# Optimization experiments

Hardware: AMD Instinct MI355X
Metric: run time of the kernel (lower is better)

## Reference

```python
import jax, jax.numpy as jnp
import numpy as np

N_ITERS = 3  # Set2Set n_iters


def _set2set(feat, gid, B, Wih, Whh, bih, bhh):
    # DGL Set2Set with n_iters=3, n_layers=1: LSTM(input=2D, hidden=D), PyTorch gate order i,f,g,o
    N, D = feat.shape
    q_star = jnp.zeros((B, 2 * D), feat.dtype)
    h = jnp.zeros((B, D), feat.dtype)
    c = jnp.zeros((B, D), feat.dtype)
    bias = bih + bhh
    for _ in range(N_ITERS):
        gates = q_star @ Wih.T + h @ Whh.T + bias  # (B, 4D)
        i, f, g, o = jnp.split(gates, 4, axis=-1)
        i = jax.nn.sigmoid(i); f = jax.nn.sigmoid(f); o = jax.nn.sigmoid(o); g = jnp.tanh(g)
        c = f * c + i * g
        h = o * jnp.tanh(c)  # q = h, shape (B, D)
        e = jnp.sum(feat * h[gid], axis=-1)  # (N,) attention logits
        m = jax.ops.segment_max(e, gid, num_segments=B, indices_are_sorted=True)
        ex = jnp.exp(e - m[gid])
        s = jax.ops.segment_sum(ex, gid, num_segments=B, indices_are_sorted=True)
        alpha = ex / s[gid]  # segment softmax
        readout = jax.ops.segment_sum(feat * alpha[:, None], gid, num_segments=B, indices_are_sorted=True)
        q_star = jnp.concatenate([h, readout], axis=-1)  # (B, 2D)
    return q_star


def setup_inputs() -> dict:
    key = jax.random.key(0)
    ks = jax.random.split(key, 18)
    N, E, D, B, OUT = 100000, 1000000, 64, 64, 1
    s = 1.0 / np.sqrt(D)
    u = lambda k, shp, b: jax.random.uniform(k, shp, jnp.float32, -b, b)
    inp = {
        'feat': jax.random.normal(ks[0], (N, D), jnp.float32),
        'efeat': jax.random.normal(ks[1], (E, D), jnp.float32),
        'edge_dst': jax.random.randint(ks[2], (E,), 0, N, jnp.int32),
        'node_graph': jnp.sort(jax.random.randint(ks[3], (N,), 0, B, jnp.int32)),
        'n_graphs': B,
        'node_Wih': u(ks[4], (4 * D, 2 * D), s), 'node_Whh': u(ks[5], (4 * D, D), s),
        'node_bih': u(ks[6], (4 * D,), s), 'node_bhh': u(ks[7], (4 * D,), s),
        'edge_Wih': u(ks[8], (4 * D, 2 * D), s), 'edge_Whh': u(ks[9], (4 * D, D), s),
        'edge_bih': u(ks[10], (4 * D,), s), 'edge_bhh': u(ks[11], (4 * D,), s),
        'W1': u(ks[12], (32, 4 * D), np.sqrt(6.0 / (4 * D + 32)) * np.sqrt(2.0)),
        'b1': jnp.zeros((32,), jnp.float32),
        'W2': u(ks[13], (16, 32), np.sqrt(6.0 / 48) * np.sqrt(2.0)),
        'b2': jnp.zeros((16,), jnp.float32),
        'W3': u(ks[14], (OUT, 16), np.sqrt(6.0 / (16 + OUT)) * np.sqrt(2.0)),
        'b3': jnp.zeros((OUT,), jnp.float32),
    }
    return inp


def reference(feat, efeat, edge_dst, node_graph, n_graphs,
              node_Wih, node_Whh, node_bih, node_bhh,
              edge_Wih, edge_Whh, edge_bih, edge_bhh,
              W1, b1, W2, b2, W3, b3):
    N = feat.shape[0]
    # mpnn = identity: node_emb = feat, edge_emb = efeat
    node_s2s = _set2set(feat, node_graph, n_graphs, node_Wih, node_Whh, node_bih, node_bhh)
    # graph.update_all(fn.copy_e, fn.mean): scatter-mean of edge features onto dst nodes
    deg = jax.ops.segment_sum(jnp.ones((efeat.shape[0],), feat.dtype), edge_dst, num_segments=N)
    edge_agg = jax.ops.segment_sum(efeat, edge_dst, num_segments=N) / jnp.maximum(deg, 1.0)[:, None]
    edge_s2s = _set2set(edge_agg, node_graph, n_graphs, edge_Wih, edge_Whh, edge_bih, edge_bhh)
    out = jnp.concatenate([node_s2s, edge_s2s], axis=1)  # (B, 4D)
    out = jax.nn.relu(out @ W1.T + b1)
    out = jax.nn.relu(out @ W2.T + b2)
    out = out @ W3.T + b3
    return out
```

## Files before the change

kernel.cpp:

```cpp
#include <hip/hip_runtime.h>
#include <math.h>

#define D 64
#define B 64
#define NPB 128
#define NSLOT 4
#define SCAN_BS 1024

__device__ __forceinline__ unsigned encf(float x) {
  unsigned u = __float_as_uint(x);
  return (u & 0x80000000u) ? ~u : (u | 0x80000000u);
}
__device__ __forceinline__ float decf(unsigned e) {
  return (e & 0x80000000u) ? __uint_as_float(e ^ 0x80000000u) : __uint_as_float(~e);
}
__device__ __forceinline__ float sigm(float x) { return 1.0f / (1.0f + __expf(-x)); }


__global__ void k_deg(const int* __restrict__ edge_dst, int* __restrict__ deg, int E) {
  int i = blockIdx.x * blockDim.x + threadIdx.x;
  if (i < E) atomicAdd(&deg[edge_dst[i]], 1);
}

__global__ void k_scan1(const int* __restrict__ deg, int* __restrict__ row_start,
                        int* __restrict__ blocksum, int N) {
  __shared__ int sm[SCAN_BS];
  int t = threadIdx.x;
  int base = blockIdx.x * SCAN_BS;
  int v = (base + t < N) ? deg[base + t] : 0;
  sm[t] = v;
  __syncthreads();
  for (int ofs = 1; ofs < SCAN_BS; ofs <<= 1) {
    int add = (t >= ofs) ? sm[t - ofs] : 0;
    __syncthreads();
    sm[t] += add;
    __syncthreads();
  }
  if (base + t < N) row_start[base + t] = sm[t] - v;
  if (t == SCAN_BS - 1) blocksum[blockIdx.x] = sm[t];
}

__global__ void k_scan2(int* __restrict__ blocksum, int nb) {
  __shared__ int sm[128];
  int t = threadIdx.x;
  int v = (t < nb) ? blocksum[t] : 0;
  sm[t] = v;
  __syncthreads();
  for (int ofs = 1; ofs < 128; ofs <<= 1) {
    int add = (t >= ofs) ? sm[t - ofs] : 0;
    __syncthreads();
    sm[t] += add;
    __syncthreads();
  }
  if (t < nb) blocksum[t] = sm[t] - v;
}

__global__ void k_scan3(int* __restrict__ row_start, const int* __restrict__ blocksum,
                        int* __restrict__ cursor, int N) {
  int n = blockIdx.x * blockDim.x + threadIdx.x;
  if (n < N) {
    int v = row_start[n] + blocksum[n / SCAN_BS];
    row_start[n] = v;
    cursor[n] = v;
  }
}

__global__ void k_fill(const int* __restrict__ edge_dst, int* __restrict__ cursor,
                       int* __restrict__ csr, int E) {
  int e = blockIdx.x * blockDim.x + threadIdx.x;
  if (e < E) {
    int dst = edge_dst[e];
    int idx = atomicAdd(&cursor[dst], 1);
    csr[idx] = e;
  }
}

__global__ void k_gather(const float* __restrict__ efeat, const int* __restrict__ csr,
                         const int* __restrict__ row_start, const int* __restrict__ deg,
                         float* __restrict__ edge_agg, int N) {
  int grp = (blockIdx.x * blockDim.x + threadIdx.x) >> 4;
  int l16 = threadIdx.x & 15;
  if (grp >= N) return;
  int base = row_start[grp];
  int dg = deg[grp];
  float4 acc = make_float4(0.f, 0.f, 0.f, 0.f);
  for (int i = 0; i < dg; i += 16) {
    int idx[16];
    #pragma unroll
    for (int j = 0; j < 16; ++j) {
      int k = i + j;
      idx[j] = csr[base + (k < dg ? k : dg - 1)];
    }
    #pragma unroll
    for (int j = 0; j < 16; ++j) {
      float4 v = *(const float4*)(efeat + (size_t)idx[j] * D + l16 * 4);
      bool ok = (i + j < dg);
      acc.x += ok ? v.x : 0.0f;
      acc.y += ok ? v.y : 0.0f;
      acc.z += ok ? v.z : 0.0f;
      acc.w += ok ? v.w : 0.0f;
    }
  }
  float inv = 1.0f / fmaxf((float)dg, 1.0f);
  acc.x *= inv; acc.y *= inv; acc.z *= inv; acc.w *= inv;
  *(float4*)(edge_agg + (size_t)grp * D + l16 * 4) = acc;
}


__global__ void k_lstm2(int first, float* __restrict__ h2, float* __restrict__ c2,
                        float* __restrict__ s2, float* __restrict__ r2,
                        unsigned* __restrict__ m2, float* __restrict__ off2,
                        const float* __restrict__ nWih, const float* __restrict__ nWhh,
                        const float* __restrict__ nbih, const float* __restrict__ nbhh,
                        const float* __restrict__ eWih, const float* __restrict__ eWhh,
                        const float* __restrict__ ebih, const float* __restrict__ ebhh) {
  __shared__ float sq[2 * D], sg[4 * D];
  int side = blockIdx.y;
  const float* Wih = side ? eWih : nWih;
  const float* Whh = side ? eWhh : nWhh;
  const float* bih = side ? ebih : nbih;
  const float* bhh = side ? ebhh : nbhh;
  float* h = h2 + side * B * D;
  float* c = c2 + side * B * D;
  float* s_buf = s2 + side * B;
  float* r_buf = r2 + side * B * D;

  int b = blockIdx.x, j = threadIdx.x;
  if (j < D) {
    sq[j] = h[b * D + j];
  } else if (j < 2 * D) {
    sq[j] = first ? 0.0f : (r_buf[b * D + (j - D)] / s_buf[b]);
  }
  __syncthreads();
  float acc = bih[j] + bhh[j];
  const float* wr = Wih + (size_t)j * (2 * D);
  #pragma unroll 8
  for (int k = 0; k < 2 * D; ++k) acc += sq[k] * wr[k];
  const float* wr2 = Whh + (size_t)j * D;
  #pragma unroll 8
  for (int k = 0; k < D; ++k) acc += sq[k] * wr2[k];
  sg[j] = acc;
  __syncthreads();
  if (j < D) {
    float ig = sigm(sg[j]);
    float fg = sigm(sg[D + j]);
    float gg = tanhf(sg[2 * D + j]);
    float og = sigm(sg[3 * D + j]);
    float cn = fg * c[b * D + j] + ig * gg;
    c[b * D + j] = cn;
    h[b * D + j] = og * tanhf(cn);
    r_buf[b * D + j] = 0.0f;
  }
  if (j == D) s_buf[b] = 0.0f;
  if (j == D + 1) {
    int idx = side * B + b;
    off2[idx] = first ? 0.0f : decf(m2[idx]);
    m2[idx] = 0u;
  }
}

__global__ void k_att_fused(const float* __restrict__ feat, const float* __restrict__ edge_agg,
                            const int* __restrict__ gid, const float* __restrict__ h2,
                            const float* __restrict__ off2, unsigned* __restrict__ m2,
                            float* __restrict__ s2, float* __restrict__ r2, int N) {
  __shared__ float r_lds[16 * NSLOT * D];
  __shared__ float s_lds[16 * NSLOT];
  __shared__ float m_lds[16 * NSLOT];
  __shared__ float h_lds[NSLOT * D];
  __shared__ float o_lds[NSLOT];
  __shared__ int sg_first;
  __shared__ int used[NSLOT];

  int side = blockIdx.y;
  const float* F = side ? edge_agg : feat;
  const float* h = h2 + side * B * D;
  const float* off = off2 + side * B;
  unsigned* m_enc = m2 + side * B;
  float* s_buf = s2 + side * B;
  float* r_buf = r2 + side * B * D;

  int tid = threadIdx.x;
  int grp = tid >> 4;
  int d4  = tid & 15;
  int base = blockIdx.x * NPB;

  for (int i = tid; i < 16 * NSLOT * D; i += 256) r_lds[i] = 0.0f;
  if (tid < 16 * NSLOT) { s_lds[tid] = 0.0f; m_lds[tid] = -3.4e38f; }
  if (tid < NSLOT) used[tid] = 0;
  if (tid == 0) sg_first = gid[base];
  __syncthreads();
  int gfirst = sg_first;
  {
    int slot = tid >> 6, dim = tid & 63;
    int g = gfirst + slot;
    if (g < B) {
      h_lds[tid] = h[g * D + dim];
      if (dim == 0) o_lds[slot] = off[g];
    }
  }
  __syncthreads();

  float4 acc = make_float4(0.f, 0.f, 0.f, 0.f);
  float sum_ex = 0.0f;
  float local_max = -3.4e38f;
  int cur_g = -1;

  for (int it = 0; it < NPB / 32; ++it) {
    int n0 = base + it * 32 + grp;
    int n1 = n0 + 16;
    bool ok0 = n0 < N, ok1 = n1 < N;
    int g0 = ok0 ? gid[n0] : -1;
    int g1 = ok1 ? gid[n1] : -1;
    float4 f0 = make_float4(0,0,0,0), f1 = make_float4(0,0,0,0);
    float dot0 = 0.f, dot1 = 0.f, ex0 = 0.f, ex1 = 0.f;
    if (ok0) {
      f0 = *(const float4*)(F + (size_t)n0 * D + d4 * 4);
      int s0 = g0 - gfirst;
      float4 hv = (s0 >= 0 && s0 < NSLOT) ? *(const float4*)&h_lds[(s0 << 6) + (d4 << 2)]
                                          : *(const float4*)(h + (size_t)g0 * D + d4 * 4);
      dot0 = f0.x * hv.x + f0.y * hv.y + f0.z * hv.z + f0.w * hv.w;
    }
    if (ok1) {
      f1 = *(const float4*)(F + (size_t)n1 * D + d4 * 4);
      int s1 = g1 - gfirst;
      float4 hv = (s1 >= 0 && s1 < NSLOT) ? *(const float4*)&h_lds[(s1 << 6) + (d4 << 2)]
                                          : *(const float4*)(h + (size_t)g1 * D + d4 * 4);
      dot1 = f1.x * hv.x + f1.y * hv.y + f1.z * hv.z + f1.w * hv.w;
    }
    dot0 += __shfl_xor(dot0, 1); dot1 += __shfl_xor(dot1, 1);
    dot0 += __shfl_xor(dot0, 2); dot1 += __shfl_xor(dot1, 2);
    dot0 += __shfl_xor(dot0, 4); dot1 += __shfl_xor(dot1, 4);
    dot0 += __shfl_xor(dot0, 8); dot1 += __shfl_xor(dot1, 8);
    if (ok0) {
      int s0 = g0 - gfirst;
      ex0 = __expf(dot0 - ((s0 >= 0 && s0 < NSLOT) ? o_lds[s0] : off[g0]));
    }
    if (ok1) {
      int s1 = g1 - gfirst;
      ex1 = __expf(dot1 - ((s1 >= 0 && s1 < NSLOT) ? o_lds[s1] : off[g1]));
    }

    #pragma unroll
    for (int pair = 0; pair < 2; ++pair) {
      bool ok = pair ? ok1 : ok0;
      int g = pair ? g1 : g0;
      float ex = pair ? ex1 : ex0;
      float dt = pair ? dot1 : dot0;
      float4 f = pair ? f1 : f0;
      if (!ok) continue;
      if (g != cur_g) {
        if (cur_g >= 0) {
          int slot = cur_g - gfirst;
          if (slot >= 0 && slot < NSLOT) {
            float4* p = (float4*)&r_lds[((grp * NSLOT + slot) << 6) + (d4 << 2)];
            float4 v = *p;
            v.x += acc.x; v.y += acc.y; v.z += acc.z; v.w += acc.w;
            *p = v;
            if (d4 == 0) {
              s_lds[grp * NSLOT + slot] += sum_ex;
              m_lds[grp * NSLOT + slot] = fmaxf(m_lds[grp * NSLOT + slot], local_max);
              used[slot] = 1;
            }
          } else {
            float* rp = r_buf + cur_g * D + d4 * 4;
            atomicAdd(rp + 0, acc.x); atomicAdd(rp + 1, acc.y);
            atomicAdd(rp + 2, acc.z); atomicAdd(rp + 3, acc.w);
            if (d4 == 0) { atomicAdd(&s_buf[cur_g], sum_ex); atomicMax(&m_enc[cur_g], encf(local_max)); }
          }
        }
        cur_g = g; acc = make_float4(0,0,0,0); sum_ex = 0.f; local_max = -3.4e38f;
      }
      acc.x += ex * f.x; acc.y += ex * f.y; acc.z += ex * f.z; acc.w += ex * f.w;
      if (d4 == 0) { sum_ex += ex; local_max = fmaxf(local_max, dt); }
    }
  }
  if (cur_g >= 0) {
    int slot = cur_g - gfirst;
    if (slot >= 0 && slot < NSLOT) {
      float4* p = (float4*)&r_lds[((grp * NSLOT + slot) << 6) + (d4 << 2)];
      float4 v = *p;
      v.x += acc.x; v.y += acc.y; v.z += acc.z; v.w += acc.w;
      *p = v;
      if (d4 == 0) {
        s_lds[grp * NSLOT + slot] += sum_ex;
        m_lds[grp * NSLOT + slot] = fmaxf(m_lds[grp * NSLOT + slot], local_max);
        used[slot] = 1;
      }
    } else {
      float* rp = r_buf + cur_g * D + d4 * 4;
      atomicAdd(rp + 0, acc.x); atomicAdd(rp + 1, acc.y);
      atomicAdd(rp + 2, acc.z); atomicAdd(rp + 3, acc.w);
      if (d4 == 0) { atomicAdd(&s_buf[cur_g], sum_ex); atomicMax(&m_enc[cur_g], encf(local_max)); }
    }
  }
  __syncthreads();

  {
    int slot = tid >> 6, dim = tid & 63;
    int g = gfirst + slot;
    if (g < B && used[slot]) {
      float sum = 0.0f;
      #pragma unroll
      for (int q = 0; q < 16; ++q) sum += r_lds[((q * NSLOT + slot) << 6) + dim];
      atomicAdd(&r_buf[g * D + dim], sum);
    }
  }
  if (tid < NSLOT) {
    int g = gfirst + tid;
    if (g < B && used[tid]) {
      float ssum = 0.0f;
      #pragma unroll
      for (int q = 0; q < 16; ++q) ssum += s_lds[q * NSLOT + tid];
      atomicAdd(&s_buf[g], ssum);
    }
  } else if (tid >= 64 && tid < 64 + NSLOT) {
    int slot = tid - 64;
    int g = gfirst + slot;
    if (g < B && used[slot]) {
      float mmax = -3.4e38f;
      #pragma unroll
      for (int q = 0; q < 16; ++q) mmax = fmaxf(mmax, m_lds[q * NSLOT + slot]);
      atomicMax(&m_enc[g], encf(mmax));
    }
  }
}

__global__ void k_mlp(const float* __restrict__ h2, const float* __restrict__ r2,
                      const float* __restrict__ s2,
                      const float* __restrict__ W1, const float* __restrict__ b1,
                      const float* __restrict__ W2, const float* __restrict__ b2,
                      const float* __restrict__ W3, const float* __restrict__ b3,
                      float* __restrict__ out) {
  __shared__ float x[4 * D], h1[32], h2s[16];
  int b = blockIdx.x, t = threadIdx.x;
  x[t]       = (t < D) ? h2[b * D + t]         : r2[b * D + (t - D)] / s2[b];
  x[128 + t] = (t < D) ? h2[B * D + b * D + t] : r2[B * D + b * D + (t - D)] / s2[B + b];
  __syncthreads();
  if (t < 32) {
    float acc = b1[t];
    const float* w = W1 + (size_t)t * (4 * D);
    #pragma unroll 8
    for (int k = 0; k < 4 * D; ++k) acc += x[k] * w[k];
    h1[t] = fmaxf(acc, 0.0f);
  }
  __syncthreads();
  if (t < 16) {
    float acc = b2[t];
    const float* w = W2 + (size_t)t * 32;
    #pragma unroll
    for (int k = 0; k < 32; ++k) acc += h1[k] * w[k];
    h2s[t] = fmaxf(acc, 0.0f);
  }
  __syncthreads();
  if (t == 0) {
    float acc = b3[0];
    #pragma unroll
    for (int k = 0; k < 16; ++k) acc += h2s[k] * W3[k];
    out[b] = acc;
  }
}


extern "C" void kernel_launch(void* const* d_in, const int* in_sizes, int n_in,
                              void* d_out, int out_size, void* d_ws, size_t ws_size,
                              hipStream_t stream) {
  const float* feat      = (const float*)d_in[0];
  const float* efeat     = (const float*)d_in[1];
  const int*   edge_dst  = (const int*)d_in[2];
  const int*   node_graph= (const int*)d_in[3];
  const float* node_Wih  = (const float*)d_in[5];
  const float* node_Whh  = (const float*)d_in[6];
  const float* node_bih  = (const float*)d_in[7];
  const float* node_bhh  = (const float*)d_in[8];
  const float* edge_Wih  = (const float*)d_in[9];
  const float* edge_Whh  = (const float*)d_in[10];
  const float* edge_bih  = (const float*)d_in[11];
  const float* edge_bhh  = (const float*)d_in[12];
  const float* W1 = (const float*)d_in[13];
  const float* b1 = (const float*)d_in[14];
  const float* W2 = (const float*)d_in[15];
  const float* b2 = (const float*)d_in[16];
  const float* W3 = (const float*)d_in[17];
  const float* b3 = (const float*)d_in[18];
  float* out = (float*)d_out;

  const int N = in_sizes[0] / D;
  const int E = in_sizes[2];

  float* ws = (float*)d_ws;
  size_t off = 0;
  float* edge_agg = ws + off; off += (size_t)N * D;
  float* h2       = ws + off; off += 2 * B * D;
  float* c2       = ws + off; off += 2 * B * D;
  float* s2       = ws + off; off += 2 * B;
  float* r2       = ws + off; off += 2 * B * D;
  float* off2     = ws + off; off += 2 * B;
  unsigned* m2    = (unsigned*)(ws + off); off += 2 * B;
  int* deg        = (int*)(ws + off); off += N;
  int* row_start  = (int*)(ws + off); off += N;
  int* cursor     = (int*)(ws + off); off += N;
  int* blocksum   = (int*)(ws + off); off += 128;
  int* csr        = (int*)(ws + off); off += E + 8;

  hipMemsetAsync(deg, 0, (size_t)N * sizeof(int), stream);
  hipMemsetAsync(h2, 0, (size_t)(4 * B * D) * sizeof(float), stream);

  const int nb = (N + SCAN_BS - 1) / SCAN_BS;
  k_deg<<<(E + 255) / 256, 256, 0, stream>>>(edge_dst, deg, E);
  k_scan1<<<nb, SCAN_BS, 0, stream>>>(deg, row_start, blocksum, N);
  k_scan2<<<1, 128, 0, stream>>>(blocksum, nb);
  k_scan3<<<(N + 255) / 256, 256, 0, stream>>>(row_start, blocksum, cursor, N);
  k_fill<<<(E + 255) / 256, 256, 0, stream>>>(edge_dst, cursor, csr, E);

  k_gather<<<(N + 15) / 16, 256, 0, stream>>>(efeat, csr, row_start, deg, edge_agg, N);

  const int att_blocks = (N + NPB - 1) / NPB;
  dim3 ga(att_blocks, 2), gb(B, 2);

  for (int it = 0; it < 3; ++it) {
    k_lstm2<<<gb, 256, 0, stream>>>(it == 0 ? 1 : 0, h2, c2, s2, r2, m2, off2,
                                    node_Wih, node_Whh, node_bih, node_bhh,
                                    edge_Wih, edge_Whh, edge_bih, edge_bhh);
    k_att_fused<<<ga, 256, 0, stream>>>(feat, edge_agg, node_graph, h2, off2, m2, s2, r2, N);
  }

  k_mlp<<<B, 128, 0, stream>>>(h2, r2, s2, W1, b1, W2, b2, W3, b3, out);
}
```

Before: 261.1 us.

## Switch edge aggregation to edge-parallel segmented reduction and fuse small setup kernels

```diff
diff --git a/kernel.cpp b/kernel.cpp
--- a/kernel.cpp
+++ b/kernel.cpp
@@ -6,6 +6,7 @@
 #define NPB 128
 #define NSLOT 4
 #define SCAN_BS 1024
+#define GR 128
 
 __device__ __forceinline__ unsigned encf(float x) {
   unsigned u = __float_as_uint(x);
@@ -17,105 +18,15 @@
 __device__ __forceinline__ float sigm(float x) { return 1.0f / (1.0f + __expf(-x)); }
 
 
-__global__ void k_deg(const int* __restrict__ edge_dst, int* __restrict__ deg, int E) {
-  int i = blockIdx.x * blockDim.x + threadIdx.x;
-  if (i < E) atomicAdd(&deg[edge_dst[i]], 1);
-}
-
-__global__ void k_scan1(const int* __restrict__ deg, int* __restrict__ row_start,
-                        int* __restrict__ blocksum, int N) {
-  __shared__ int sm[SCAN_BS];
-  int t = threadIdx.x;
-  int base = blockIdx.x * SCAN_BS;
-  int v = (base + t < N) ? deg[base + t] : 0;
-  sm[t] = v;
-  __syncthreads();
-  for (int ofs = 1; ofs < SCAN_BS; ofs <<= 1) {
-    int add = (t >= ofs) ? sm[t - ofs] : 0;
-    __syncthreads();
-    sm[t] += add;
-    __syncthreads();
-  }
-  if (base + t < N) row_start[base + t] = sm[t] - v;
-  if (t == SCAN_BS - 1) blocksum[blockIdx.x] = sm[t];
-}
-
-__global__ void k_scan2(int* __restrict__ blocksum, int nb) {
-  __shared__ int sm[128];
-  int t = threadIdx.x;
-  int v = (t < nb) ? blocksum[t] : 0;
-  sm[t] = v;
-  __syncthreads();
-  for (int ofs = 1; ofs < 128; ofs <<= 1) {
-    int add = (t >= ofs) ? sm[t - ofs] : 0;
-    __syncthreads();
-    sm[t] += add;
-    __syncthreads();
-  }
-  if (t < nb) blocksum[t] = sm[t] - v;
-}
-
-__global__ void k_scan3(int* __restrict__ row_start, const int* __restrict__ blocksum,
-                        int* __restrict__ cursor, int N) {
-  int n = blockIdx.x * blockDim.x + threadIdx.x;
-  if (n < N) {
-    int v = row_start[n] + blocksum[n / SCAN_BS];
-    row_start[n] = v;
-    cursor[n] = v;
-  }
-}
-
-__global__ void k_fill(const int* __restrict__ edge_dst, int* __restrict__ cursor,
-                       int* __restrict__ csr, int E) {
-  int e = blockIdx.x * blockDim.x + threadIdx.x;
-  if (e < E) {
-    int dst = edge_dst[e];
-    int idx = atomicAdd(&cursor[dst], 1);
-    csr[idx] = e;
-  }
-}
-
-__global__ void k_gather(const float* __restrict__ efeat, const int* __restrict__ csr,
-                         const int* __restrict__ row_start, const int* __restrict__ deg,
-                         float* __restrict__ edge_agg, int N) {
-  int grp = (blockIdx.x * blockDim.x + threadIdx.x) >> 4;
-  int l16 = threadIdx.x & 15;
-  if (grp >= N) return;
-  int base = row_start[grp];
-  int dg = deg[grp];
-  float4 acc = make_float4(0.f, 0.f, 0.f, 0.f);
-  for (int i = 0; i < dg; i += 16) {
-    int idx[16];
-    #pragma unroll
-    for (int j = 0; j < 16; ++j) {
-      int k = i + j;
-      idx[j] = csr[base + (k < dg ? k : dg - 1)];
-    }
-    #pragma unroll
-    for (int j = 0; j < 16; ++j) {
-      float4 v = *(const float4*)(efeat + (size_t)idx[j] * D + l16 * 4);
-      bool ok = (i + j < dg);
-      acc.x += ok ? v.x : 0.0f;
-      acc.y += ok ? v.y : 0.0f;
-      acc.z += ok ? v.z : 0.0f;
-      acc.w += ok ? v.w : 0.0f;
-    }
-  }
-  float inv = 1.0f / fmaxf((float)dg, 1.0f);
-  acc.x *= inv; acc.y *= inv; acc.z *= inv; acc.w *= inv;
-  *(float4*)(edge_agg + (size_t)grp * D + l16 * 4) = acc;
-}
-
-
-__global__ void k_lstm2(int first, float* __restrict__ h2, float* __restrict__ c2,
-                        float* __restrict__ s2, float* __restrict__ r2,
-                        unsigned* __restrict__ m2, float* __restrict__ off2,
-                        const float* __restrict__ nWih, const float* __restrict__ nWhh,
-                        const float* __restrict__ nbih, const float* __restrict__ nbhh,
-                        const float* __restrict__ eWih, const float* __restrict__ eWhh,
-                        const float* __restrict__ ebih, const float* __restrict__ ebhh) {
-  __shared__ float sq[2 * D], sg[4 * D];
-  int side = blockIdx.y;
+__device__ __forceinline__ void lstm_body(int side, int b, int first,
+    float* __restrict__ h2, float* __restrict__ c2,
+    float* __restrict__ s2, float* __restrict__ r2,
+    unsigned* __restrict__ m2, float* __restrict__ off2,
+    const float* __restrict__ nWih, const float* __restrict__ nWhh,
+    const float* __restrict__ nbih, const float* __restrict__ nbhh,
+    const float* __restrict__ eWih, const float* __restrict__ eWhh,
+    const float* __restrict__ ebih, const float* __restrict__ ebhh,
+    float* sq, float* sg) {
   const float* Wih = side ? eWih : nWih;
   const float* Whh = side ? eWhh : nWhh;
   const float* bih = side ? ebih : nbih;
@@ -125,7 +36,7 @@
   float* s_buf = s2 + side * B;
   float* r_buf = r2 + side * B * D;
 
-  int b = blockIdx.x, j = threadIdx.x;
+  int j = threadIdx.x;
   if (j < D) {
     sq[j] = h[b * D + j];
   } else if (j < 2 * D) {
@@ -158,6 +69,150 @@
     m2[idx] = 0u;
   }
 }
+
+
+__global__ void k_deg_lstm(int DEG, const int* __restrict__ edge_dst, int* __restrict__ deg, int E,
+                           float* __restrict__ h2, float* __restrict__ c2,
+                           float* __restrict__ s2, float* __restrict__ r2,
+                           unsigned* __restrict__ m2, float* __restrict__ off2,
+                           const float* __restrict__ nWih, const float* __restrict__ nWhh,
+                           const float* __restrict__ nbih, const float* __restrict__ nbhh,
+                           const float* __restrict__ eWih, const float* __restrict__ eWhh,
+                           const float* __restrict__ ebih, const float* __restrict__ ebhh) {
+  __shared__ float sq[2 * D], sg[4 * D];
+  int bx = blockIdx.x;
+  if (bx < DEG) {
+    int i = bx * 256 + threadIdx.x;
+    if (i < E) atomicAdd(&deg[edge_dst[i]], 1);
+  } else {
+    int j = bx - DEG;
+    lstm_body(j >> 6, j & 63, 1, h2, c2, s2, r2, m2, off2,
+              nWih, nWhh, nbih, nbhh, eWih, eWhh, ebih, ebhh, sq, sg);
+  }
+}
+
+__global__ void k_scan1(const int* __restrict__ deg, int* __restrict__ row_start,
+                        int* __restrict__ blocksum, int N) {
+  __shared__ int sm[SCAN_BS];
+  int t = threadIdx.x;
+  int base = blockIdx.x * SCAN_BS;
+  int v = (base + t < N) ? deg[base + t] : 0;
+  sm[t] = v;
+  __syncthreads();
+  for (int ofs = 1; ofs < SCAN_BS; ofs <<= 1) {
+    int add = (t >= ofs) ? sm[t - ofs] : 0;
+    __syncthreads();
+    sm[t] += add;
+    __syncthreads();
+  }
+  if (base + t < N) row_start[base + t] = sm[t] - v;
+  if (t == SCAN_BS - 1) blocksum[blockIdx.x] = sm[t];
+}
+
+__global__ void k_scan3(int* __restrict__ row_start, const int* __restrict__ blocksum,
+                        int* __restrict__ cursor, int N, int nb) {
+  __shared__ int sm[128];
+  int t = threadIdx.x;
+  if (t < 128) sm[t] = (t < nb) ? blocksum[t] : 0;
+  __syncthreads();
+  for (int ofs = 1; ofs < 128; ofs <<= 1) {
+    int add = (t < 128 && t >= ofs) ? sm[t - ofs] : 0;
+    __syncthreads();
+    if (t < 128) sm[t] += add;
+    __syncthreads();
+  }
+  int n = blockIdx.x * 256 + t;
+  if (n < N) {
+    int c = n / SCAN_BS;
+    int v = row_start[n] + ((c > 0) ? sm[c - 1] : 0);
+    row_start[n] = v;
+    cursor[n] = v;
+  }
+}
+
+__global__ void k_fill(const int* __restrict__ edge_dst, int* __restrict__ cursor,
+                       int* __restrict__ csr, int* __restrict__ csr_dst, int E) {
+  int e = blockIdx.x * blockDim.x + threadIdx.x;
+  if (e < E) {
+    int dst = edge_dst[e];
+    int idx = atomicAdd(&cursor[dst], 1);
+    csr[idx] = e;
+    csr_dst[idx] = dst;
+  }
+}
+
+__global__ void k_gather(const float* __restrict__ efeat, const int* __restrict__ csr,
+                         const int* __restrict__ csr_dst, float* __restrict__ edge_agg, int E) {
+  __shared__ int s_id[4 * GR], s_d[4 * GR];
+  int tid = threadIdx.x;
+  int bbase = blockIdx.x * (4 * GR);
+  #pragma unroll
+  for (int q = 0; q < 2; ++q) {
+    int p = tid + q * 256;
+    int gi = bbase + p;
+    if (gi < E) { s_id[p] = csr[gi]; s_d[p] = csr_dst[gi]; }
+    else        { s_id[p] = 0;       s_d[p] = -1; }
+  }
+  __syncthreads();
+  int wave = tid >> 6, lane = tid & 63;
+  int wbase = wave * GR;
+  float acc = 0.0f;
+  int cur = s_d[wbase];
+  bool firstSeg = true;
+  for (int j8 = 0; j8 < GR; j8 += 8) {
+    float v[8]; int d[8];
+    #pragma unroll
+    for (int jj = 0; jj < 8; ++jj) {
+      int p = wbase + j8 + jj;
+      d[jj] = s_d[p];
+      v[jj] = efeat[(size_t)s_id[p] * D + lane];
+    }
+    #pragma unroll
+    for (int jj = 0; jj < 8; ++jj) {
+      if (d[jj] != cur) {
+        if (cur >= 0) {
+          if (firstSeg) atomicAdd(&edge_agg[(size_t)cur * D + lane], acc);
+          else          edge_agg[(size_t)cur * D + lane] = acc;
+        }
+        firstSeg = false;
+        cur = d[jj];
+        acc = 0.0f;
+      }
+      acc += (d[jj] >= 0) ? v[jj] : 0.0f;
+    }
+  }
+  if (cur >= 0) atomicAdd(&edge_agg[(size_t)cur * D + lane], acc);
+}
+
+__global__ void k_div(float* __restrict__ edge_agg, const int* __restrict__ deg, int N) {
+  int idx = blockIdx.x * blockDim.x + threadIdx.x;
+  int n = idx >> 4, l16 = idx & 15;
+  if (n >= N) return;
+  int dg = deg[n];
+  float4* p = (float4*)(edge_agg + (size_t)n * D + l16 * 4);
+  if (dg > 0) {
+    float inv = 1.0f / (float)dg;
+    float4 v = *p;
+    v.x *= inv; v.y *= inv; v.z *= inv; v.w *= inv;
+    *p = v;
+  } else {
+    *p = make_float4(0.f, 0.f, 0.f, 0.f);
+  }
+}
+
+
+__global__ void k_lstm2(int first, float* __restrict__ h2, float* __restrict__ c2,
+                        float* __restrict__ s2, float* __restrict__ r2,
+                        unsigned* __restrict__ m2, float* __restrict__ off2,
+                        const float* __restrict__ nWih, const float* __restrict__ nWhh,
+                        const float* __restrict__ nbih, const float* __restrict__ nbhh,
+                        const float* __restrict__ eWih, const float* __restrict__ eWhh,
+                        const float* __restrict__ ebih, const float* __restrict__ ebhh) {
+  __shared__ float sq[2 * D], sg[4 * D];
+  lstm_body(blockIdx.y, blockIdx.x, first, h2, c2, s2, r2, m2, off2,
+            nWih, nWhh, nbih, nbhh, eWih, eWhh, ebih, ebhh, sq, sg);
+}
+
 
 __global__ void k_att_fused(const float* __restrict__ feat, const float* __restrict__ edge_agg,
                             const int* __restrict__ gid, const float* __restrict__ h2,
@@ -325,6 +380,7 @@
   }
 }
 
+
 __global__ void k_mlp(const float* __restrict__ h2, const float* __restrict__ r2,
                       const float* __restrict__ s2,
                       const float* __restrict__ W1, const float* __restrict__ b1,
@@ -392,33 +448,39 @@
   float* edge_agg = ws + off; off += (size_t)N * D;
   float* h2       = ws + off; off += 2 * B * D;
   float* c2       = ws + off; off += 2 * B * D;
+  int* deg        = (int*)(ws + off); off += N;
   float* s2       = ws + off; off += 2 * B;
   float* r2       = ws + off; off += 2 * B * D;
   float* off2     = ws + off; off += 2 * B;
   unsigned* m2    = (unsigned*)(ws + off); off += 2 * B;
-  int* deg        = (int*)(ws + off); off += N;
   int* row_start  = (int*)(ws + off); off += N;
   int* cursor     = (int*)(ws + off); off += N;
   int* blocksum   = (int*)(ws + off); off += 128;
   int* csr        = (int*)(ws + off); off += E + 8;
-
-  hipMemsetAsync(deg, 0, (size_t)N * sizeof(int), stream);
-  hipMemsetAsync(h2, 0, (size_t)(4 * B * D) * sizeof(float), stream);
-
-  const int nb = (N + SCAN_BS - 1) / SCAN_BS;
-  k_deg<<<(E + 255) / 256, 256, 0, stream>>>(edge_dst, deg, E);
+  int* csr_dst    = (int*)(ws + off); off += E + 8;
+
+  hipMemsetAsync(ws, 0, ((size_t)N * D + 4 * B * D + N) * sizeof(float), stream);
+
+  const int nb  = (N + SCAN_BS - 1) / SCAN_BS;
+  const int DEG = (E + 255) / 256;
+  const int ATT = (N + NPB - 1) / NPB;
+
+  k_deg_lstm<<<DEG + 128, 256, 0, stream>>>(DEG, edge_dst, deg, E, h2, c2, s2, r2, m2, off2,
+      node_Wih, node_Whh, node_bih, node_bhh, edge_Wih, edge_Whh, edge_bih, edge_bhh);
   k_scan1<<<nb, SCAN_BS, 0, stream>>>(deg, row_start, blocksum, N);
-  k_scan2<<<1, 128, 0, stream>>>(blocksum, nb);
-  k_scan3<<<(N + 255) / 256, 256, 0, stream>>>(row_start, blocksum, cursor, N);
-  k_fill<<<(E + 255) / 256, 256, 0, stream>>>(edge_dst, cursor, csr, E);
-
-  k_gather<<<(N + 15) / 16, 256, 0, stream>>>(efeat, csr, row_start, deg, edge_agg, N);
-
-  const int att_blocks = (N + NPB - 1) / NPB;
-  dim3 ga(att_blocks, 2), gb(B, 2);
-
-  for (int it = 0; it < 3; ++it) {
-    k_lstm2<<<gb, 256, 0, stream>>>(it == 0 ? 1 : 0, h2, c2, s2, r2, m2, off2,
+  k_scan3<<<(N + 255) / 256, 256, 0, stream>>>(row_start, blocksum, cursor, N, nb);
+  k_fill<<<DEG, 256, 0, stream>>>(edge_dst, cursor, csr, csr_dst, E);
+
+  k_gather<<<(E + 4 * GR - 1) / (4 * GR), 256, 0, stream>>>(efeat, csr, csr_dst, edge_agg, E);
+  {
+    long long tot = (long long)N * 16;
+    k_div<<<(int)((tot + 255) / 256), 256, 0, stream>>>(edge_agg, deg, N);
+  }
+
+  dim3 ga(ATT, 2), gb(B, 2);
+  k_att_fused<<<ga, 256, 0, stream>>>(feat, edge_agg, node_graph, h2, off2, m2, s2, r2, N);
+  for (int it = 1; it < 3; ++it) {
+    k_lstm2<<<gb, 256, 0, stream>>>(0, h2, c2, s2, r2, m2, off2,
                                     node_Wih, node_Whh, node_bih, node_bhh,
                                     edge_Wih, edge_Whh, edge_bih, edge_bhh);
     k_att_fused<<<ga, 256, 0, stream>>>(feat, edge_agg, node_graph, h2, off2, m2, s2, r2, N);
```

Measured after the change: 278.9 us. 1.07x slower.

## Fuse first LSTM step into degree kernel, merge scans, use register segment accumulators

Applied to the files above, without the earlier changes.

```diff
diff --git a/kernel.cpp b/kernel.cpp
--- a/kernel.cpp
+++ b/kernel.cpp
@@ -17,9 +17,77 @@
 __device__ __forceinline__ float sigm(float x) { return 1.0f / (1.0f + __expf(-x)); }
 
 
-__global__ void k_deg(const int* __restrict__ edge_dst, int* __restrict__ deg, int E) {
-  int i = blockIdx.x * blockDim.x + threadIdx.x;
-  if (i < E) atomicAdd(&deg[edge_dst[i]], 1);
+__device__ __forceinline__ void lstm_body(int side, int b, int first,
+    float* __restrict__ h2, float* __restrict__ c2,
+    float* __restrict__ s2, float* __restrict__ r2,
+    unsigned* __restrict__ m2, float* __restrict__ off2,
+    const float* __restrict__ nWih, const float* __restrict__ nWhh,
+    const float* __restrict__ nbih, const float* __restrict__ nbhh,
+    const float* __restrict__ eWih, const float* __restrict__ eWhh,
+    const float* __restrict__ ebih, const float* __restrict__ ebhh,
+    float* sq, float* sg) {
+  const float* Wih = side ? eWih : nWih;
+  const float* Whh = side ? eWhh : nWhh;
+  const float* bih = side ? ebih : nbih;
+  const float* bhh = side ? ebhh : nbhh;
+  float* h = h2 + side * B * D;
+  float* c = c2 + side * B * D;
+  float* s_buf = s2 + side * B;
+  float* r_buf = r2 + side * B * D;
+
+  int j = threadIdx.x;
+  if (j < D) {
+    sq[j] = h[b * D + j];
+  } else if (j < 2 * D) {
+    sq[j] = first ? 0.0f : (r_buf[b * D + (j - D)] / s_buf[b]);
+  }
+  __syncthreads();
+  float acc = bih[j] + bhh[j];
+  const float* wr = Wih + (size_t)j * (2 * D);
+  #pragma unroll 8
+  for (int k = 0; k < 2 * D; ++k) acc += sq[k] * wr[k];
+  const float* wr2 = Whh + (size_t)j * D;
+  #pragma unroll 8
+  for (int k = 0; k < D; ++k) acc += sq[k] * wr2[k];
+  sg[j] = acc;
+  __syncthreads();
+  if (j < D) {
+    float ig = sigm(sg[j]);
+    float fg = sigm(sg[D + j]);
+    float gg = tanhf(sg[2 * D + j]);
+    float og = sigm(sg[3 * D + j]);
+    float cn = fg * c[b * D + j] + ig * gg;
+    c[b * D + j] = cn;
+    h[b * D + j] = og * tanhf(cn);
+    r_buf[b * D + j] = 0.0f;
+  }
+  if (j == D) s_buf[b] = 0.0f;
+  if (j == D + 1) {
+    int idx = side * B + b;
+    off2[idx] = first ? 0.0f : decf(m2[idx]);
+    m2[idx] = 0u;
+  }
+}
+
+
+__global__ void k_deg_lstm(int DEG, const int* __restrict__ edge_dst, int* __restrict__ deg, int E,
+                           float* __restrict__ h2, float* __restrict__ c2,
+                           float* __restrict__ s2, float* __restrict__ r2,
+                           unsigned* __restrict__ m2, float* __restrict__ off2,
+                           const float* __restrict__ nWih, const float* __restrict__ nWhh,
+                           const float* __restrict__ nbih, const float* __restrict__ nbhh,
+                           const float* __restrict__ eWih, const float* __restrict__ eWhh,
+                           const float* __restrict__ ebih, const float* __restrict__ ebhh) {
+  __shared__ float sq[2 * D], sg[4 * D];
+  int bx = blockIdx.x;
+  if (bx < DEG) {
+    int i = bx * 256 + threadIdx.x;
+    if (i < E) atomicAdd(&deg[edge_dst[i]], 1);
+  } else {
+    int j = bx - DEG;
+    lstm_body(j >> 6, j & 63, 1, h2, c2, s2, r2, m2, off2,
+              nWih, nWhh, nbih, nbhh, eWih, eWhh, ebih, ebhh, sq, sg);
+  }
 }
 
 __global__ void k_scan1(const int* __restrict__ deg, int* __restrict__ row_start,
@@ -40,26 +108,22 @@
   if (t == SCAN_BS - 1) blocksum[blockIdx.x] = sm[t];
 }
 
-__global__ void k_scan2(int* __restrict__ blocksum, int nb) {
+__global__ void k_scan3(int* __restrict__ row_start, const int* __restrict__ blocksum,
+                        int* __restrict__ cursor, int N, int nb) {
   __shared__ int sm[128];
   int t = threadIdx.x;
-  int v = (t < nb) ? blocksum[t] : 0;
-  sm[t] = v;
+  if (t < 128) sm[t] = (t < nb) ? blocksum[t] : 0;
   __syncthreads();
   for (int ofs = 1; ofs < 128; ofs <<= 1) {
-    int add = (t >= ofs) ? sm[t - ofs] : 0;
+    int add = (t < 128 && t >= ofs) ? sm[t - ofs] : 0;
     __syncthreads();
-    sm[t] += add;
+    if (t < 128) sm[t] += add;
     __syncthreads();
   }
-  if (t < nb) blocksum[t] = sm[t] - v;
-}
-
-__global__ void k_scan3(int* __restrict__ row_start, const int* __restrict__ blocksum,
-                        int* __restrict__ cursor, int N) {
-  int n = blockIdx.x * blockDim.x + threadIdx.x;
+  int n = blockIdx.x * 256 + t;
   if (n < N) {
-    int v = row_start[n] + blocksum[n / SCAN_BS];
+    int c = n / SCAN_BS;
+    int v = row_start[n] + ((c > 0) ? sm[c - 1] : 0);
     row_start[n] = v;
     cursor[n] = v;
   }
@@ -74,6 +138,7 @@
     csr[idx] = e;
   }
 }
+
 
 __global__ void k_gather(const float* __restrict__ efeat, const int* __restrict__ csr,
                          const int* __restrict__ row_start, const int* __restrict__ deg,
@@ -115,61 +180,21 @@
                         const float* __restrict__ eWih, const float* __restrict__ eWhh,
                         const float* __restrict__ ebih, const float* __restrict__ ebhh) {
   __shared__ float sq[2 * D], sg[4 * D];
-  int side = blockIdx.y;
-  const float* Wih = side ? eWih : nWih;
-  const float* Whh = side ? eWhh : nWhh;
-  const float* bih = side ? ebih : nbih;
-  const float* bhh = side ? ebhh : nbhh;
-  float* h = h2 + side * B * D;
-  float* c = c2 + side * B * D;
-  float* s_buf = s2 + side * B;
-  float* r_buf = r2 + side * B * D;
-
-  int b = blockIdx.x, j = threadIdx.x;
-  if (j < D) {
-    sq[j] = h[b * D + j];
-  } else if (j < 2 * D) {
-    sq[j] = first ? 0.0f : (r_buf[b * D + (j - D)] / s_buf[b]);
-  }
-  __syncthreads();
-  float acc = bih[j] + bhh[j];
-  const float* wr = Wih + (size_t)j * (2 * D);
-  #pragma unroll 8
-  for (int k = 0; k < 2 * D; ++k) acc += sq[k] * wr[k];
-  const float* wr2 = Whh + (size_t)j * D;
-  #pragma unroll 8
-  for (int k = 0; k < D; ++k) acc += sq[k] * wr2[k];
-  sg[j] = acc;
-  __syncthreads();
-  if (j < D) {
-    float ig = sigm(sg[j]);
-    float fg = sigm(sg[D + j]);
-    float gg = tanhf(sg[2 * D + j]);
-    float og = sigm(sg[3 * D + j]);
-    float cn = fg * c[b * D + j] + ig * gg;
-    c[b * D + j] = cn;
-    h[b * D + j] = og * tanhf(cn);
-    r_buf[b * D + j] = 0.0f;
-  }
-  if (j == D) s_buf[b] = 0.0f;
-  if (j == D + 1) {
-    int idx = side * B + b;
-    off2[idx] = first ? 0.0f : decf(m2[idx]);
-    m2[idx] = 0u;
-  }
-}
+  lstm_body(blockIdx.y, blockIdx.x, first, h2, c2, s2, r2, m2, off2,
+            nWih, nWhh, nbih, nbhh, eWih, eWhh, ebih, ebhh, sq, sg);
+}
+
 
 __global__ void k_att_fused(const float* __restrict__ feat, const float* __restrict__ edge_agg,
                             const int* __restrict__ gid, const float* __restrict__ h2,
                             const float* __restrict__ off2, unsigned* __restrict__ m2,
                             float* __restrict__ s2, float* __restrict__ r2, int N) {
-  __shared__ float r_lds[16 * NSLOT * D];
-  __shared__ float s_lds[16 * NSLOT];
-  __shared__ float m_lds[16 * NSLOT];
   __shared__ float h_lds[NSLOT * D];
   __shared__ float o_lds[NSLOT];
-  __shared__ int sg_first;
-  __shared__ int used[NSLOT];
+  __shared__ float r_lds[4][NSLOT][D];
+  __shared__ float s_lds[4][NSLOT];
+  __shared__ float m_lds[4][NSLOT];
+  __shared__ int sg_first, sg_count;
 
   int side = blockIdx.y;
   const float* F = side ? edge_agg : feat;
@@ -182,28 +207,50 @@
   int tid = threadIdx.x;
   int grp = tid >> 4;
   int d4  = tid & 15;
+  int wave = tid >> 6;
+  int lane = tid & 63;
   int base = blockIdx.x * NPB;
 
-  for (int i = tid; i < 16 * NSLOT * D; i += 256) r_lds[i] = 0.0f;
-  if (tid < 16 * NSLOT) { s_lds[tid] = 0.0f; m_lds[tid] = -3.4e38f; }
-  if (tid < NSLOT) used[tid] = 0;
-  if (tid == 0) sg_first = gid[base];
-  __syncthreads();
-  int gfirst = sg_first;
+  if (tid == 0) {
+    int gf = gid[base];
+    sg_first = gf;
+    sg_count = gid[min(base + NPB, N) - 1] - gf + 1;
+  }
+  __syncthreads();
+  const int gfirst = sg_first;
+  const int gcount = sg_count;
   {
     int slot = tid >> 6, dim = tid & 63;
     int g = gfirst + slot;
-    if (g < B) {
-      h_lds[tid] = h[g * D + dim];
+    if (slot < NSLOT && g < B) {
+      h_lds[slot * D + dim] = h[g * D + dim];
       if (dim == 0) o_lds[slot] = off[g];
     }
   }
   __syncthreads();
 
-  float4 acc = make_float4(0.f, 0.f, 0.f, 0.f);
-  float sum_ex = 0.0f;
-  float local_max = -3.4e38f;
+  float4 a0 = make_float4(0,0,0,0), a1 = a0, a2 = a0, a3 = a0;
+  float se0 = 0.f, se1 = 0.f, se2 = 0.f, se3 = 0.f;
+  float mx0 = -3.4e38f, mx1 = mx0, mx2 = mx0, mx3 = mx0;
+  float4 acc = make_float4(0,0,0,0);
+  float sum_ex = 0.f, local_max = -3.4e38f;
   int cur_g = -1;
+
+#define FLUSH_SEG() do { \
+    if (cur_g >= 0) { \
+      int s_ = cur_g - gfirst; \
+      if (s_ == 0)      { a0.x+=acc.x; a0.y+=acc.y; a0.z+=acc.z; a0.w+=acc.w; se0+=sum_ex; mx0=fmaxf(mx0,local_max); } \
+      else if (s_ == 1) { a1.x+=acc.x; a1.y+=acc.y; a1.z+=acc.z; a1.w+=acc.w; se1+=sum_ex; mx1=fmaxf(mx1,local_max); } \
+      else if (s_ == 2) { a2.x+=acc.x; a2.y+=acc.y; a2.z+=acc.z; a2.w+=acc.w; se2+=sum_ex; mx2=fmaxf(mx2,local_max); } \
+      else if (s_ == 3) { a3.x+=acc.x; a3.y+=acc.y; a3.z+=acc.z; a3.w+=acc.w; se3+=sum_ex; mx3=fmaxf(mx3,local_max); } \
+      else { \
+        float* rp = r_buf + cur_g * D + d4 * 4; \
+        atomicAdd(rp+0,acc.x); atomicAdd(rp+1,acc.y); atomicAdd(rp+2,acc.z); atomicAdd(rp+3,acc.w); \
+        if (d4 == 0) { atomicAdd(&s_buf[cur_g],sum_ex); atomicMax(&m_enc[cur_g],encf(local_max)); } \
+      } \
+    } \
+    acc = make_float4(0,0,0,0); sum_ex = 0.f; local_max = -3.4e38f; \
+  } while(0)
 
   for (int it = 0; it < NPB / 32; ++it) {
     int n0 = base + it * 32 + grp;
@@ -240,90 +287,69 @@
       ex1 = __expf(dot1 - ((s1 >= 0 && s1 < NSLOT) ? o_lds[s1] : off[g1]));
     }
 
-    #pragma unroll
-    for (int pair = 0; pair < 2; ++pair) {
-      bool ok = pair ? ok1 : ok0;
-      int g = pair ? g1 : g0;
-      float ex = pair ? ex1 : ex0;
-      float dt = pair ? dot1 : dot0;
-      float4 f = pair ? f1 : f0;
-      if (!ok) continue;
-      if (g != cur_g) {
-        if (cur_g >= 0) {
-          int slot = cur_g - gfirst;
-          if (slot >= 0 && slot < NSLOT) {
-            float4* p = (float4*)&r_lds[((grp * NSLOT + slot) << 6) + (d4 << 2)];
-            float4 v = *p;
-            v.x += acc.x; v.y += acc.y; v.z += acc.z; v.w += acc.w;
-            *p = v;
-            if (d4 == 0) {
-              s_lds[grp * NSLOT + slot] += sum_ex;
-              m_lds[grp * NSLOT + slot] = fmaxf(m_lds[grp * NSLOT + slot], local_max);
-              used[slot] = 1;
-            }
-          } else {
-            float* rp = r_buf + cur_g * D + d4 * 4;
-            atomicAdd(rp + 0, acc.x); atomicAdd(rp + 1, acc.y);
-            atomicAdd(rp + 2, acc.z); atomicAdd(rp + 3, acc.w);
-            if (d4 == 0) { atomicAdd(&s_buf[cur_g], sum_ex); atomicMax(&m_enc[cur_g], encf(local_max)); }
-          }
-        }
-        cur_g = g; acc = make_float4(0,0,0,0); sum_ex = 0.f; local_max = -3.4e38f;
-      }
-      acc.x += ex * f.x; acc.y += ex * f.y; acc.z += ex * f.z; acc.w += ex * f.w;
-      if (d4 == 0) { sum_ex += ex; local_max = fmaxf(local_max, dt); }
-    }
-  }
-  if (cur_g >= 0) {
-    int slot = cur_g - gfirst;
-    if (slot >= 0 && slot < NSLOT) {
-      float4* p = (float4*)&r_lds[((grp * NSLOT + slot) << 6) + (d4 << 2)];
-      float4 v = *p;
-      v.x += acc.x; v.y += acc.y; v.z += acc.z; v.w += acc.w;
-      *p = v;
-      if (d4 == 0) {
-        s_lds[grp * NSLOT + slot] += sum_ex;
-        m_lds[grp * NSLOT + slot] = fmaxf(m_lds[grp * NSLOT + slot], local_max);
-        used[slot] = 1;
-      }
-    } else {
-      float* rp = r_buf + cur_g * D + d4 * 4;
-      atomicAdd(rp + 0, acc.x); atomicAdd(rp + 1, acc.y);
-      atomicAdd(rp + 2, acc.z); atomicAdd(rp + 3, acc.w);
-      if (d4 == 0) { atomicAdd(&s_buf[cur_g], sum_ex); atomicMax(&m_enc[cur_g], encf(local_max)); }
-    }
+    if (ok0) {
+      if (g0 != cur_g) { FLUSH_SEG(); cur_g = g0; }
+      acc.x += ex0 * f0.x; acc.y += ex0 * f0.y; acc.z += ex0 * f0.z; acc.w += ex0 * f0.w;
+      if (d4 == 0) { sum_ex += ex0; local_max = fmaxf(local_max, dot0); }
+    }
+    if (ok1) {
+      if (g1 != cur_g) { FLUSH_SEG(); cur_g = g1; }
+      acc.x += ex1 * f1.x; acc.y += ex1 * f1.y; acc.z += ex1 * f1.z; acc.w += ex1 * f1.w;
+      if (d4 == 0) { sum_ex += ex1; local_max = fmaxf(local_max, dot1); }
+    }
+  }
+  FLUSH_SEG();
+#undef FLUSH_SEG
+
+#define WRED4(A) \
+    A.x += __shfl_xor(A.x, 16); A.y += __shfl_xor(A.y, 16); A.z += __shfl_xor(A.z, 16); A.w += __shfl_xor(A.w, 16); \
+    A.x += __shfl_xor(A.x, 32); A.y += __shfl_xor(A.y, 32); A.z += __shfl_xor(A.z, 32); A.w += __shfl_xor(A.w, 32);
+#define WRED1(S) S += __shfl_xor(S, 16); S += __shfl_xor(S, 32);
+#define WREDM(M) M = fmaxf(M, __shfl_xor(M, 16)); M = fmaxf(M, __shfl_xor(M, 32));
+
+  WRED4(a0); WRED1(se0); WREDM(mx0);
+  if (gcount > 1) { WRED4(a1); WRED1(se1); WREDM(mx1); }
+  if (gcount > 2) { WRED4(a2); WRED1(se2); WREDM(mx2); }
+  if (gcount > 3) { WRED4(a3); WRED1(se3); WREDM(mx3); }
+#undef WRED4
+#undef WRED1
+#undef WREDM
+
+  if (lane < 16) {
+    *(float4*)&r_lds[wave][0][lane * 4] = a0;
+    if (gcount > 1) *(float4*)&r_lds[wave][1][lane * 4] = a1;
+    if (gcount > 2) *(float4*)&r_lds[wave][2][lane * 4] = a2;
+    if (gcount > 3) *(float4*)&r_lds[wave][3][lane * 4] = a3;
+  }
+  if (lane == 0) {
+    s_lds[wave][0] = se0; m_lds[wave][0] = mx0;
+    if (gcount > 1) { s_lds[wave][1] = se1; m_lds[wave][1] = mx1; }
+    if (gcount > 2) { s_lds[wave][2] = se2; m_lds[wave][2] = mx2; }
+    if (gcount > 3) { s_lds[wave][3] = se3; m_lds[wave][3] = mx3; }
   }
   __syncthreads();
 
   {
     int slot = tid >> 6, dim = tid & 63;
     int g = gfirst + slot;
-    if (g < B && used[slot]) {
-      float sum = 0.0f;
-      #pragma unroll
-      for (int q = 0; q < 16; ++q) sum += r_lds[((q * NSLOT + slot) << 6) + dim];
+    if (slot < gcount && g < B) {
+      float sum = r_lds[0][slot][dim] + r_lds[1][slot][dim]
+                + r_lds[2][slot][dim] + r_lds[3][slot][dim];
       atomicAdd(&r_buf[g * D + dim], sum);
     }
   }
-  if (tid < NSLOT) {
+  if (tid < NSLOT && tid < gcount) {
     int g = gfirst + tid;
-    if (g < B && used[tid]) {
-      float ssum = 0.0f;
-      #pragma unroll
-      for (int q = 0; q < 16; ++q) ssum += s_lds[q * NSLOT + tid];
+    if (g < B) {
+      float ssum = s_lds[0][tid] + s_lds[1][tid] + s_lds[2][tid] + s_lds[3][tid];
       atomicAdd(&s_buf[g], ssum);
-    }
-  } else if (tid >= 64 && tid < 64 + NSLOT) {
-    int slot = tid - 64;
-    int g = gfirst + slot;
-    if (g < B && used[slot]) {
-      float mmax = -3.4e38f;
-      #pragma unroll
-      for (int q = 0; q < 16; ++q) mmax = fmaxf(mmax, m_lds[q * NSLOT + slot]);
-      atomicMax(&m_enc[g], encf(mmax));
-    }
-  }
-}
+      float mm = fmaxf(fmaxf(m_lds[0][tid], m_lds[1][tid]),
+                       fmaxf(m_lds[2][tid], m_lds[3][tid]));
+      atomicMax(&m_enc[g], encf(mm));
+    }
+  }
+}
+
 
 __global__ void k_mlp(const float* __restrict__ h2, const float* __restrict__ r2,
                       const float* __restrict__ s2,
@@ -389,36 +415,37 @@
 
   float* ws = (float*)d_ws;
   size_t off = 0;
-  float* edge_agg = ws + off; off += (size_t)N * D;
+  int* deg        = (int*)(ws + off); off += N;
   float* h2       = ws + off; off += 2 * B * D;
   float* c2       = ws + off; off += 2 * B * D;
+  float* edge_agg = ws + off; off += (size_t)N * D;
   float* s2       = ws + off; off += 2 * B;
   float* r2       = ws + off; off += 2 * B * D;
   float* off2     = ws + off; off += 2 * B;
   unsigned* m2    = (unsigned*)(ws + off); off += 2 * B;
-  int* deg        = (int*)(ws + off); off += N;
   int* row_start  = (int*)(ws + off); off += N;
   int* cursor     = (int*)(ws + off); off += N;
   int* blocksum   = (int*)(ws + off); off += 128;
   int* csr        = (int*)(ws + off); off += E + 8;
 
-  hipMemsetAsync(deg, 0, (size_t)N * sizeof(int), stream);
-  hipMemsetAsync(h2, 0, (size_t)(4 * B * D) * sizeof(float), stream);
-
-  const int nb = (N + SCAN_BS - 1) / SCAN_BS;
-  k_deg<<<(E + 255) / 256, 256, 0, stream>>>(edge_dst, deg, E);
+  hipMemsetAsync(ws, 0, ((size_t)N + 4 * B * D) * sizeof(float), stream);
+
+  const int nb  = (N + SCAN_BS - 1) / SCAN_BS;
+  const int DEG = (E + 255) / 256;
+  const int ATT = (N + NPB - 1) / NPB;
+
+  k_deg_lstm<<<DEG + 128, 256, 0, stream>>>(DEG, edge_dst, deg, E, h2, c2, s2, r2, m2, off2,
+      node_Wih, node_Whh, node_bih, node_bhh, edge_Wih, edge_Whh, edge_bih, edge_bhh);
   k_scan1<<<nb, SCAN_BS, 0, stream>>>(deg, row_start, blocksum, N);
-  k_scan2<<<1, 128, 0, stream>>>(blocksum, nb);
-  k_scan3<<<(N + 255) / 256, 256, 0, stream>>>(row_start, blocksum, cursor, N);
-  k_fill<<<(E + 255) / 256, 256, 0, stream>>>(edge_dst, cursor, csr, E);
+  k_scan3<<<(N + 255) / 256, 256, 0, stream>>>(row_start, blocksum, cursor, N, nb);
+  k_fill<<<DEG, 256, 0, stream>>>(edge_dst, cursor, csr, E);
 
   k_gather<<<(N + 15) / 16, 256, 0, stream>>>(efeat, csr, row_start, deg, edge_agg, N);
 
-  const int att_blocks = (N + NPB - 1) / NPB;
-  dim3 ga(att_blocks, 2), gb(B, 2);
-
-  for (int it = 0; it < 3; ++it) {
-    k_lstm2<<<gb, 256, 0, stream>>>(it == 0 ? 1 : 0, h2, c2, s2, r2, m2, off2,
+  dim3 ga(ATT, 2), gb(B, 2);
+  k_att_fused<<<ga, 256, 0, stream>>>(feat, edge_agg, node_graph, h2, off2, m2, s2, r2, N);
+  for (int it = 1; it < 3; ++it) {
+    k_lstm2<<<gb, 256, 0, stream>>>(0, h2, c2, s2, r2, m2, off2,
                                     node_Wih, node_Whh, node_bih, node_bhh,
                                     edge_Wih, edge_Whh, edge_bih, edge_bhh);
     k_att_fused<<<ga, 256, 0, stream>>>(feat, edge_agg, node_graph, h2, off2, m2, s2, r2, N);
```

After: 276.9 us. 1.06x slower.
